# Kernel optimization log

Hardware: AMD Instinct MI355X
Metric: run time of the kernel (lower is better)

Reference implementation:

```python
import jax, jax.numpy as jnp
import numpy as np

HEADS = 4
DIM_HEAD = 32
SCALE = DIM_HEAD ** -0.5
EPS = 1e-5


def setup_inputs() -> dict:
    key = jax.random.key(0)
    k1, k2, k3, k4 = jax.random.split(key, 4)
    dim = 256
    hidden = HEADS * DIM_HEAD  # 128
    x = jax.random.normal(k1, (16, dim, 64, 64), dtype=jnp.float32)
    # 1x1 conv weights stored as [out_ch, in_ch] (kernel size 1 squeezed)
    w_qkv = jax.random.normal(k2, (hidden * 3, dim), dtype=jnp.float32) * (dim ** -0.5)
    w_out = jax.random.normal(k3, (dim, hidden), dtype=jnp.float32) * (hidden ** -0.5)
    b_out = jax.random.normal(k4, (dim,), dtype=jnp.float32) * 0.01
    g = jnp.ones((1, dim, 1, 1), dtype=jnp.float32)  # LayerNorm gain
    return {"x": x, "w_qkv": w_qkv, "w_out": w_out, "b_out": b_out, "g": g}


def reference(x, w_qkv, w_out, b_out, g):
    b, c, h, w = x.shape
    n = h * w
    # 1x1 conv to qkv: [b, 3*hidden, h, w]
    qkv = jnp.einsum('oc,bchw->bohw', w_qkv, x)
    q, k, v = jnp.split(qkv, 3, axis=1)

    def to_heads(t):
        return t.reshape(b, HEADS, DIM_HEAD, n)  # b h d n

    q, k, v = to_heads(q), to_heads(k), to_heads(v)
    q = jax.nn.softmax(q, axis=2) * SCALE       # softmax over head-dim d
    k = jax.nn.softmax(k, axis=3)               # softmax over spatial n
    v = v / n                                    # v / (h*w)
    context = jnp.einsum('bhdn,bhen->bhde', k, v)
    out = jnp.einsum('bhde,bhdn->bhen', context, q)  # b h e n
    out = out.reshape(b, HEADS * DIM_HEAD, h, w)
    # output 1x1 conv with bias
    out = jnp.einsum('oc,bchw->bohw', w_out, out) + b_out[None, :, None, None]
    # channel LayerNorm (biased variance over dim=1)
    mean = jnp.mean(out, axis=1, keepdims=True)
    var = jnp.var(out, axis=1, keepdims=True)
    return (out - mean) * jax.lax.rsqrt(var + EPS) * g
```

## Files before the change

kernel.cpp:

```cpp
#include <hip/hip_runtime.h>

typedef short short8 __attribute__((ext_vector_type(8)));
typedef float f32x16 __attribute__((ext_vector_type(16)));
typedef unsigned short ushort_t;

#define B_    16
#define C_    256
#define N_    4096
#define H_    4
#define HID_  128
#define SCALE_ 0.17677669529663687f
#define EPS_  1e-5f

__device__ inline ushort_t f2bf(float f) {
  union { float f; unsigned u; } a; a.f = f;
  unsigned r = a.u + 0x7FFFu + ((a.u >> 16) & 1u);
  return (ushort_t)(r >> 16);
}

__device__ inline int2 pack4(float a, float b, float c, float d) {
  int2 o;
  o.x = (int)f2bf(a) | ((int)f2bf(b) << 16);
  o.y = (int)f2bf(c) | ((int)f2bf(d) << 16);
  return o;
}

__device__ inline short8 ld_frag16(const ushort_t* p) {
  return __builtin_bit_cast(short8, *(const int4*)p);
}
__device__ inline short8 ld_frag8(const ushort_t* p) {
  int2 a = *(const int2*)p, b = *(const int2*)(p + 4);
  int4 t; t.x = a.x; t.y = a.y; t.z = b.x; t.w = b.y;
  return __builtin_bit_cast(short8, t);
}

__global__ void k0_wswz(const float* __restrict__ w, ushort_t* __restrict__ wsw) {
  int gid = blockIdx.x * 256 + threadIdx.x;
  int ln = gid & 63, kc = (gid >> 6) & 15, mt = gid >> 10;
  int row = mt * 32 + (ln & 31);
  int col = kc * 16 + (ln >> 5) * 8;
  const float* src = w + (size_t)row * 256 + col;
  float4 a = *(const float4*)src, b = *(const float4*)(src + 4);
  union { ushort_t u[8]; int4 v; } o;
  o.u[0] = f2bf(a.x); o.u[1] = f2bf(a.y); o.u[2] = f2bf(a.z); o.u[3] = f2bf(a.w);
  o.u[4] = f2bf(b.x); o.u[5] = f2bf(b.y); o.u[6] = f2bf(b.z); o.u[7] = f2bf(b.w);
  *(int4*)(wsw + (size_t)gid * 8) = o.v;
}

__global__ __launch_bounds__(512, 4) void k1_qkv(
    const float* __restrict__ x, const ushort_t* __restrict__ wsw,
    ushort_t* __restrict__ qp, float* __restrict__ pctx, float* __restrict__ psum)
{
  __shared__ __align__(16) union {
    ushort_t Xs[64 * 264];
    struct { ushort_t kt[128 * 68]; ushort_t vt[128 * 68]; } s2;
  } sm;

  const int tid = threadIdx.x;
  const int b = blockIdx.y;
  const int blk = blockIdx.x;
  const int n0 = blk * 64;
  const int w = tid >> 6, lane = tid & 63;
  const int half = lane >> 5, lm = lane & 31;
  const int hw = w >> 1, ntile = w & 1;
  const int gnt = blk * 2 + ntile;

  {
    const float* xsrc = x + (size_t)b * C_ * N_ + n0;
    const int n4 = tid & 15;
    const int cqA = tid >> 4;
    const int cqB = cqA + 32;
    const float* pA = xsrc + (size_t)(cqA * 4) * N_ + n4 * 4;
    const float* pB = xsrc + (size_t)(cqB * 4) * N_ + n4 * 4;
    float4 a0 = *(const float4*)(pA);
    float4 a1 = *(const float4*)(pA + N_);
    float4 a2 = *(const float4*)(pA + 2 * N_);
    float4 a3 = *(const float4*)(pA + 3 * N_);
    float4 b0 = *(const float4*)(pB);
    float4 b1 = *(const float4*)(pB + N_);
    float4 b2 = *(const float4*)(pB + 2 * N_);
    float4 b3 = *(const float4*)(pB + 3 * N_);
    ushort_t* dA = sm.Xs + (((cqA >> 1) ^ n4) * 8 + (cqA & 1) * 4) + (n4 * 4) * 264;
    ushort_t* dB = sm.Xs + (((cqB >> 1) ^ n4) * 8 + (cqB & 1) * 4) + (n4 * 4) * 264;
    *(int2*)(dA + 0 * 264) = pack4(a0.x, a1.x, a2.x, a3.x);
    *(int2*)(dA + 1 * 264) = pack4(a0.y, a1.y, a2.y, a3.y);
    *(int2*)(dA + 2 * 264) = pack4(a0.z, a1.z, a2.z, a3.z);
    *(int2*)(dA + 3 * 264) = pack4(a0.w, a1.w, a2.w, a3.w);
    *(int2*)(dB + 0 * 264) = pack4(b0.x, b1.x, b2.x, b3.x);
    *(int2*)(dB + 1 * 264) = pack4(b0.y, b1.y, b2.y, b3.y);
    *(int2*)(dB + 2 * 264) = pack4(b0.z, b1.z, b2.z, b3.z);
    *(int2*)(dB + 3 * 264) = pack4(b0.w, b1.w, b2.w, b3.w);
  }
  __syncthreads();

  f32x16 acc0, acc1, acc2;
  for (int r = 0; r < 16; ++r) { acc0[r] = 0.0f; acc1[r] = 0.0f; acc2[r] = 0.0f; }
  {
    const ushort_t* xrow = sm.Xs + (ntile * 32 + lm) * 264;
    const int sn = ntile * 8 + (lm >> 2);
    for (int kc = 0; kc < 16; ++kc) {
      short8 bfrag = ld_frag16(xrow + (((2 * kc + half) ^ sn) << 3));
      short8 af0 = ld_frag16(wsw + (size_t)(((hw) * 16 + kc) * 64 + lane) * 8);
      short8 af1 = ld_frag16(wsw + (size_t)(((4 + hw) * 16 + kc) * 64 + lane) * 8);
      short8 af2 = ld_frag16(wsw + (size_t)(((8 + hw) * 16 + kc) * 64 + lane) * 8);
      acc0 = __builtin_amdgcn_mfma_f32_32x32x16_bf16(af0, bfrag, acc0, 0, 0, 0);
      acc1 = __builtin_amdgcn_mfma_f32_32x32x16_bf16(af1, bfrag, acc1, 0, 0, 0);
      acc2 = __builtin_amdgcn_mfma_f32_32x32x16_bf16(af2, bfrag, acc2, 0, 0, 0);
    }
  }

  {
    float m = -1e30f;
    for (int r = 0; r < 16; ++r) m = fmaxf(m, acc0[r]);
    m = fmaxf(m, __shfl_xor(m, 32));
    float s = 0.0f;
    for (int r = 0; r < 16; ++r) s += __expf(acc0[r] - m);
    s += __shfl_xor(s, 32);
    float sc = SCALE_ / s;
    ushort_t* qpb = qp + (size_t)b * N_ * 128;
    for (int q = 0; q < 4; ++q) {
      int kc = hw * 2 + (q >> 1);
      int fl = (q & 1) * 32 + lm;
      float v0 = __expf(acc0[q * 4 + 0] - m) * sc;
      float v1 = __expf(acc0[q * 4 + 1] - m) * sc;
      float v2 = __expf(acc0[q * 4 + 2] - m) * sc;
      float v3 = __expf(acc0[q * 4 + 3] - m) * sc;
      int2 o;
      o.x = (int)f2bf(v0) | ((int)f2bf(v1) << 16);
      o.y = (int)f2bf(v2) | ((int)f2bf(v3) << 16);
      *(int2*)(qpb + (size_t)((gnt * 8 + kc) * 64 + fl) * 8 + 4 * half) = o;
    }
  }

  float ev[16];
  for (int r = 0; r < 16; ++r) ev[r] = __expf(acc1[r]);

  __syncthreads();

  for (int r = 0; r < 16; ++r) {
    int row = (r & 3) + 8 * (r >> 2) + 4 * half;
    sm.s2.kt[(hw * 32 + row) * 68 + ntile * 32 + lm] = f2bf(ev[r]);
    sm.s2.vt[(hw * 32 + row) * 68 + ntile * 32 + lm] = f2bf(acc2[r]);
  }

  for (int mask = 1; mask <= 16; mask <<= 1)
    for (int r = 0; r < 16; ++r) ev[r] += __shfl_xor(ev[r], mask);
  if (lm == 0) {
    float* ps = psum + ((size_t)(b * 4 + hw) * 128 + gnt) * 32;
    for (int r = 0; r < 16; ++r) {
      int row = (r & 3) + 8 * (r >> 2) + 4 * half;
      ps[row] = ev[r];
    }
  }
  __syncthreads();

  if (ntile == 0) {
    f32x16 cacc;
    for (int r = 0; r < 16; ++r) cacc[r] = 0.0f;
    const ushort_t* ka = sm.s2.kt + (hw * 32 + lm) * 68 + half * 8;
    const ushort_t* va = sm.s2.vt + (hw * 32 + lm) * 68 + half * 8;
    for (int s = 0; s < 4; ++s) {
      short8 af = ld_frag8(ka + s * 16);
      short8 bf = ld_frag8(va + s * 16);
      cacc = __builtin_amdgcn_mfma_f32_32x32x16_bf16(af, bf, cacc, 0, 0, 0);
    }
    float* pc = pctx + ((size_t)(b * 4 + hw) * 64 + blk) * 1024;
    for (int r = 0; r < 16; ++r) {
      int row = (r & 3) + 8 * (r >> 2) + 4 * half;
      pc[row * 32 + lm] = cacc[r];
    }
  }
}

__global__ __launch_bounds__(256) void k2b_weff(
    const float* __restrict__ pctx, const float* __restrict__ psum,
    const float* __restrict__ wout, ushort_t* __restrict__ weff)
{
  __shared__ float ctxs[32][32];
  __shared__ float inv[32];
  const int tid = threadIdx.x;
  const int ph = blockIdx.x, pb = blockIdx.y;
  const size_t bh = (size_t)(pb * 4 + ph);
  if (tid < 32) {
    float s = 0.0f;
    const float* ps = psum + bh * 128 * 32 + tid;
    #pragma unroll 8
    for (int c = 0; c < 128; ++c) s += ps[c * 32];
    inv[tid] = 1.0f / (s * 4096.0f);
  }
  __syncthreads();
  {
    float4 s4 = make_float4(0.f, 0.f, 0.f, 0.f);
    const float* pc = pctx + bh * 64 * 1024 + tid * 4;
    #pragma unroll 8
    for (int c = 0; c < 64; ++c) {
      float4 v = *(const float4*)(pc + c * 1024);
      s4.x += v.x; s4.y += v.y; s4.z += v.z; s4.w += v.w;
    }
    int d = tid >> 3;
    float iv = inv[d];
    float* crow = &ctxs[0][0] + tid * 4;
    crow[0] = s4.x * iv; crow[1] = s4.y * iv; crow[2] = s4.z * iv; crow[3] = s4.w * iv;
  }
  __syncthreads();
  {
    const int oc = tid;
    const int mt = oc >> 5, lmm = oc & 31;
    const float* wrow = wout + (size_t)oc * HID_ + ph * 32;
    float wr[32];
    for (int e = 0; e < 32; ++e) wr[e] = wrow[e];
    float vals[32];
    for (int d = 0; d < 32; ++d) {
      float s = 0.0f;
      for (int e = 0; e < 32; ++e) s += wr[e] * ctxs[d][e];
      vals[d] = s;
    }
    ushort_t* wb_b = weff + (size_t)pb * 32768;
    for (int kci = 0; kci < 2; ++kci) {
      int kc = ph * 2 + kci;
      for (int hf = 0; hf < 2; ++hf) {
        int d0 = kci * 16 + hf * 8;
        union { ushort_t u[8]; int4 v; } o;
        for (int j = 0; j < 8; ++j) o.u[j] = f2bf(vals[d0 + j]);
        *(int4*)(wb_b + (size_t)((mt * 8 + kc) * 64 + hf * 32 + lmm) * 8) = o.v;
      }
    }
  }
}

__global__ __launch_bounds__(256, 4) void k3_out(
    const ushort_t* __restrict__ weff, const ushort_t* __restrict__ qp,
    const float* __restrict__ bout, const float* __restrict__ g,
    float* __restrict__ out)
{
  __shared__ float part_s[2][64], part_s2[2][64];
  __shared__ float st_mu[64], st_rs[64];

  const int tid = threadIdx.x;
  const int b = blockIdx.y;
  const int blk = blockIdx.x;
  const int n0 = blk * 64;
  const int w = tid >> 6, lane = tid & 63;
  const int half = lane >> 5, lm = lane & 31;
  const int ntile = w & 1, mgrp = w >> 1;
  const int gnt = blk * 2 + ntile;

  f32x16 acc[4];
  for (int i = 0; i < 4; ++i)
    for (int r = 0; r < 16; ++r) acc[i][r] = 0.0f;

  {
    const ushort_t* qb = qp + (size_t)b * N_ * 128 + (size_t)gnt * 8 * 64 * 8;
    const ushort_t* wbase = weff + (size_t)b * 32768 + ((size_t)(mgrp * 4) * 8 * 64 + lane) * 8;
    for (int kc = 0; kc < 8; ++kc) {
      short8 bfrag = ld_frag16(qb + (size_t)(kc * 64 + lane) * 8);
      for (int i = 0; i < 4; ++i) {
        short8 af = ld_frag16(wbase + (size_t)((i * 8 + kc) * 64) * 8);
        acc[i] = __builtin_amdgcn_mfma_f32_32x32x16_bf16(af, bfrag, acc[i], 0, 0, 0);
      }
    }
  }

  float s = 0.0f, s2v = 0.0f;
  for (int i = 0; i < 4; ++i) {
    int mt = mgrp * 4 + i;
    for (int r = 0; r < 16; ++r) {
      int row = mt * 32 + (r & 3) + 8 * (r >> 2) + 4 * half;
      acc[i][r] += bout[row];
      float v = acc[i][r];
      s += v; s2v += v * v;
    }
  }
  s += __shfl_xor(s, 32);
  s2v += __shfl_xor(s2v, 32);
  if (half == 0) { part_s[mgrp][ntile * 32 + lm] = s; part_s2[mgrp][ntile * 32 + lm] = s2v; }
  __syncthreads();
  if (tid < 64) {
    float S = part_s[0][tid] + part_s[1][tid];
    float S2 = part_s2[0][tid] + part_s2[1][tid];
    float mu = S * (1.0f / 256.0f);
    float var = S2 * (1.0f / 256.0f) - mu * mu;
    st_mu[tid] = mu;
    st_rs[tid] = rsqrtf(var + EPS_);
  }
  __syncthreads();

  const int col = ntile * 32 + lm;
  const float mu = st_mu[col];
  const float rs = st_rs[col];
  float* ob = out + (size_t)b * C_ * N_ + n0 + col;
  for (int i = 0; i < 4; ++i) {
    int mt = mgrp * 4 + i;
    for (int r = 0; r < 16; ++r) {
      int row = mt * 32 + (r & 3) + 8 * (r >> 2) + 4 * half;
      ob[(size_t)row * N_] = (acc[i][r] - mu) * rs * g[row];
    }
  }
}

extern "C" void kernel_launch(void* const* d_in, const int* in_sizes, int n_in,
                              void* d_out, int out_size, void* d_ws, size_t ws_size,
                              hipStream_t stream) {
  (void)in_sizes; (void)n_in; (void)out_size; (void)ws_size;
  const float* x    = (const float*)d_in[0];
  const float* wqkv = (const float*)d_in[1];
  const float* wout = (const float*)d_in[2];
  const float* bout = (const float*)d_in[3];
  const float* g    = (const float*)d_in[4];
  float* out = (float*)d_out;

  char* ws = (char*)d_ws;
  ushort_t* qp   = (ushort_t*)(ws);
  float*    pctx = (float*)(ws + ((size_t)16 << 20));
  float*    psum = (float*)(ws + ((size_t)32 << 20));
  ushort_t* weff = (ushort_t*)(ws + ((size_t)33 << 20));
  ushort_t* wsw  = (ushort_t*)(ws + ((size_t)34 << 20));

  k0_wswz<<<48, 256, 0, stream>>>(wqkv, wsw);
  k1_qkv<<<dim3(64, 16), 512, 0, stream>>>(x, wsw, qp, pctx, psum);
  k2b_weff<<<dim3(4, 16), 256, 0, stream>>>(pctx, psum, wout, weff);
  k3_out<<<dim3(64, 16), 256, 0, stream>>>(weff, qp, bout, g, out);
}
```

Baseline: 168.0 us.

## Reduce context and key sums with global atomics and software-pipeline QKV loads

```diff
diff --git a/kernel.cpp b/kernel.cpp
--- a/kernel.cpp
+++ b/kernel.cpp
@@ -34,8 +34,16 @@
   return __builtin_bit_cast(short8, t);
 }
 
-__global__ void k0_wswz(const float* __restrict__ w, ushort_t* __restrict__ wsw) {
+__global__ void k0_wswz(const float* __restrict__ w, ushort_t* __restrict__ wsw,
+                        float* __restrict__ ctxg, float* __restrict__ psumg) {
   int gid = blockIdx.x * 256 + threadIdx.x;
+  #pragma unroll
+  for (int i = 0; i < 6; ++i) {
+    int idx = gid + i * 12288;
+    if (idx < 65536) ctxg[idx] = 0.0f;
+  }
+  if (gid < 2048) psumg[gid] = 0.0f;
+
   int ln = gid & 63, kc = (gid >> 6) & 15, mt = gid >> 10;
   int row = mt * 32 + (ln & 31);
   int col = kc * 16 + (ln >> 5) * 8;
@@ -49,7 +57,7 @@
 
 __global__ __launch_bounds__(512, 4) void k1_qkv(
     const float* __restrict__ x, const ushort_t* __restrict__ wsw,
-    ushort_t* __restrict__ qp, float* __restrict__ pctx, float* __restrict__ psum)
+    ushort_t* __restrict__ qp, float* __restrict__ ctxg, float* __restrict__ psumg)
 {
   __shared__ __align__(16) union {
     ushort_t Xs[64 * 264];
@@ -98,36 +106,46 @@
   {
     const ushort_t* xrow = sm.Xs + (ntile * 32 + lm) * 264;
     const int sn = ntile * 8 + (lm >> 2);
+    const ushort_t* wl = wsw + (size_t)(hw * 16 * 64 + lane) * 8;
+
+#define LOADK(kc, BF, A0, A1, A2) \
+    BF = ld_frag16(xrow + (((2 * (kc) + half) ^ sn) << 3)); \
+    A0 = ld_frag16(wl + (kc) * 512); \
+    A1 = ld_frag16(wl + 32768 + (kc) * 512); \
+    A2 = ld_frag16(wl + 65536 + (kc) * 512);
+
+    short8 cb, c0, c1, c2, nb, n0f, n1f, n2f;
+    LOADK(0, cb, c0, c1, c2);
+    LOADK(1, nb, n0f, n1f, n2f);
+    #pragma unroll
     for (int kc = 0; kc < 16; ++kc) {
-      short8 bfrag = ld_frag16(xrow + (((2 * kc + half) ^ sn) << 3));
-      short8 af0 = ld_frag16(wsw + (size_t)(((hw) * 16 + kc) * 64 + lane) * 8);
-      short8 af1 = ld_frag16(wsw + (size_t)(((4 + hw) * 16 + kc) * 64 + lane) * 8);
-      short8 af2 = ld_frag16(wsw + (size_t)(((8 + hw) * 16 + kc) * 64 + lane) * 8);
-      acc0 = __builtin_amdgcn_mfma_f32_32x32x16_bf16(af0, bfrag, acc0, 0, 0, 0);
-      acc1 = __builtin_amdgcn_mfma_f32_32x32x16_bf16(af1, bfrag, acc1, 0, 0, 0);
-      acc2 = __builtin_amdgcn_mfma_f32_32x32x16_bf16(af2, bfrag, acc2, 0, 0, 0);
-    }
+      short8 tb, t0, t1, t2;
+      if (kc < 14) { LOADK(kc + 2, tb, t0, t1, t2); }
+      else { tb = cb; t0 = c0; t1 = c1; t2 = c2; }
+      acc0 = __builtin_amdgcn_mfma_f32_32x32x16_bf16(c0, cb, acc0, 0, 0, 0);
+      acc1 = __builtin_amdgcn_mfma_f32_32x32x16_bf16(c1, cb, acc1, 0, 0, 0);
+      acc2 = __builtin_amdgcn_mfma_f32_32x32x16_bf16(c2, cb, acc2, 0, 0, 0);
+      cb = nb; c0 = n0f; c1 = n1f; c2 = n2f;
+      nb = tb; n0f = t0; n1f = t1; n2f = t2;
+    }
+#undef LOADK
   }
 
   {
     float m = -1e30f;
     for (int r = 0; r < 16; ++r) m = fmaxf(m, acc0[r]);
     m = fmaxf(m, __shfl_xor(m, 32));
+    float qe[16];
     float s = 0.0f;
-    for (int r = 0; r < 16; ++r) s += __expf(acc0[r] - m);
+    for (int r = 0; r < 16; ++r) { qe[r] = __expf(acc0[r] - m); s += qe[r]; }
     s += __shfl_xor(s, 32);
     float sc = SCALE_ / s;
     ushort_t* qpb = qp + (size_t)b * N_ * 128;
     for (int q = 0; q < 4; ++q) {
       int kc = hw * 2 + (q >> 1);
       int fl = (q & 1) * 32 + lm;
-      float v0 = __expf(acc0[q * 4 + 0] - m) * sc;
-      float v1 = __expf(acc0[q * 4 + 1] - m) * sc;
-      float v2 = __expf(acc0[q * 4 + 2] - m) * sc;
-      float v3 = __expf(acc0[q * 4 + 3] - m) * sc;
-      int2 o;
-      o.x = (int)f2bf(v0) | ((int)f2bf(v1) << 16);
-      o.y = (int)f2bf(v2) | ((int)f2bf(v3) << 16);
+      int2 o = pack4(qe[q * 4 + 0] * sc, qe[q * 4 + 1] * sc,
+                     qe[q * 4 + 2] * sc, qe[q * 4 + 3] * sc);
       *(int2*)(qpb + (size_t)((gnt * 8 + kc) * 64 + fl) * 8 + 4 * half) = o;
     }
   }
@@ -142,38 +160,40 @@
     sm.s2.kt[(hw * 32 + row) * 68 + ntile * 32 + lm] = f2bf(ev[r]);
     sm.s2.vt[(hw * 32 + row) * 68 + ntile * 32 + lm] = f2bf(acc2[r]);
   }
-
-  for (int mask = 1; mask <= 16; mask <<= 1)
-    for (int r = 0; r < 16; ++r) ev[r] += __shfl_xor(ev[r], mask);
-  if (lm == 0) {
-    float* ps = psum + ((size_t)(b * 4 + hw) * 128 + gnt) * 32;
-    for (int r = 0; r < 16; ++r) {
-      int row = (r & 3) + 8 * (r >> 2) + 4 * half;
-      ps[row] = ev[r];
-    }
-  }
-  __syncthreads();
-
-  if (ntile == 0) {
-    f32x16 cacc;
-    for (int r = 0; r < 16; ++r) cacc[r] = 0.0f;
-    const ushort_t* ka = sm.s2.kt + (hw * 32 + lm) * 68 + half * 8;
-    const ushort_t* va = sm.s2.vt + (hw * 32 + lm) * 68 + half * 8;
-    for (int s = 0; s < 4; ++s) {
+  __syncthreads();
+
+  {
+    f32x16 cacc, sacc;
+    for (int r = 0; r < 16; ++r) { cacc[r] = 0.0f; sacc[r] = 0.0f; }
+    short8 ones;
+    #pragma unroll
+    for (int j = 0; j < 8; ++j) ones[j] = (short)0x3F80;
+    const ushort_t* ka = sm.s2.kt + (hw * 32 + lm) * 68 + ntile * 32 + half * 8;
+    const ushort_t* va = sm.s2.vt + (hw * 32 + lm) * 68 + ntile * 32 + half * 8;
+    #pragma unroll
+    for (int s = 0; s < 2; ++s) {
       short8 af = ld_frag8(ka + s * 16);
       short8 bf = ld_frag8(va + s * 16);
       cacc = __builtin_amdgcn_mfma_f32_32x32x16_bf16(af, bf, cacc, 0, 0, 0);
-    }
-    float* pc = pctx + ((size_t)(b * 4 + hw) * 64 + blk) * 1024;
+      sacc = __builtin_amdgcn_mfma_f32_32x32x16_bf16(af, ones, sacc, 0, 0, 0);
+    }
+    float* pc = ctxg + (size_t)(b * 4 + hw) * 1024;
     for (int r = 0; r < 16; ++r) {
       int row = (r & 3) + 8 * (r >> 2) + 4 * half;
-      pc[row * 32 + lm] = cacc[r];
+      atomicAdd(pc + row * 32 + lm, cacc[r]);
+    }
+    if (lm == 0) {
+      float* ps = psumg + (size_t)(b * 4 + hw) * 32;
+      for (int r = 0; r < 16; ++r) {
+        int row = (r & 3) + 8 * (r >> 2) + 4 * half;
+        atomicAdd(ps + row, sacc[r]);
+      }
     }
   }
 }
 
 __global__ __launch_bounds__(256) void k2b_weff(
-    const float* __restrict__ pctx, const float* __restrict__ psum,
+    const float* __restrict__ ctxg, const float* __restrict__ psumg,
     const float* __restrict__ wout, ushort_t* __restrict__ weff)
 {
   __shared__ float ctxs[32][32];
@@ -181,26 +201,13 @@
   const int tid = threadIdx.x;
   const int ph = blockIdx.x, pb = blockIdx.y;
   const size_t bh = (size_t)(pb * 4 + ph);
-  if (tid < 32) {
-    float s = 0.0f;
-    const float* ps = psum + bh * 128 * 32 + tid;
-    #pragma unroll 8
-    for (int c = 0; c < 128; ++c) s += ps[c * 32];
-    inv[tid] = 1.0f / (s * 4096.0f);
-  }
-  __syncthreads();
-  {
-    float4 s4 = make_float4(0.f, 0.f, 0.f, 0.f);
-    const float* pc = pctx + bh * 64 * 1024 + tid * 4;
-    #pragma unroll 8
-    for (int c = 0; c < 64; ++c) {
-      float4 v = *(const float4*)(pc + c * 1024);
-      s4.x += v.x; s4.y += v.y; s4.z += v.z; s4.w += v.w;
-    }
-    int d = tid >> 3;
-    float iv = inv[d];
+  float4 v = *(const float4*)(ctxg + bh * 1024 + tid * 4);
+  if (tid < 32) inv[tid] = 1.0f / (psumg[bh * 32 + tid] * 4096.0f);
+  __syncthreads();
+  {
+    float iv = inv[tid >> 3];
     float* crow = &ctxs[0][0] + tid * 4;
-    crow[0] = s4.x * iv; crow[1] = s4.y * iv; crow[2] = s4.z * iv; crow[3] = s4.w * iv;
+    crow[0] = v.x * iv; crow[1] = v.y * iv; crow[2] = v.z * iv; crow[3] = v.w * iv;
   }
   __syncthreads();
   {
@@ -311,13 +318,13 @@
 
   char* ws = (char*)d_ws;
   ushort_t* qp   = (ushort_t*)(ws);
-  float*    pctx = (float*)(ws + ((size_t)16 << 20));
-  float*    psum = (float*)(ws + ((size_t)32 << 20));
-  ushort_t* weff = (ushort_t*)(ws + ((size_t)33 << 20));
-  ushort_t* wsw  = (ushort_t*)(ws + ((size_t)34 << 20));
-
-  k0_wswz<<<48, 256, 0, stream>>>(wqkv, wsw);
-  k1_qkv<<<dim3(64, 16), 512, 0, stream>>>(x, wsw, qp, pctx, psum);
-  k2b_weff<<<dim3(4, 16), 256, 0, stream>>>(pctx, psum, wout, weff);
+  ushort_t* weff = (ushort_t*)(ws + ((size_t)16 << 20));
+  ushort_t* wsw  = (ushort_t*)(ws + ((size_t)17 << 20));
+  float*    ctxg = (float*)(ws + ((size_t)18 << 20));
+  float*    psumg= (float*)(ws + ((size_t)18 << 20) + (256 << 10));
+
+  k0_wswz<<<48, 256, 0, stream>>>(wqkv, wsw, ctxg, psumg);
+  k1_qkv<<<dim3(64, 16), 512, 0, stream>>>(x, wsw, qp, ctxg, psumg);
+  k2b_weff<<<dim3(4, 16), 256, 0, stream>>>(ctxg, psumg, wout, weff);
   k3_out<<<dim3(64, 16), 256, 0, stream>>>(weff, qp, bout, g, out);
 }
```

Measured after the change: 230.2 us. 37.1% more time.

## Split partial context reduction into a separate wide-grid kernel, cache q exponentials

Applied to the files above, without the earlier changes.

```diff
diff --git a/kernel.cpp b/kernel.cpp
--- a/kernel.cpp
+++ b/kernel.cpp
@@ -113,21 +113,17 @@
     float m = -1e30f;
     for (int r = 0; r < 16; ++r) m = fmaxf(m, acc0[r]);
     m = fmaxf(m, __shfl_xor(m, 32));
+    float qe[16];
     float s = 0.0f;
-    for (int r = 0; r < 16; ++r) s += __expf(acc0[r] - m);
+    for (int r = 0; r < 16; ++r) { qe[r] = __expf(acc0[r] - m); s += qe[r]; }
     s += __shfl_xor(s, 32);
     float sc = SCALE_ / s;
     ushort_t* qpb = qp + (size_t)b * N_ * 128;
     for (int q = 0; q < 4; ++q) {
       int kc = hw * 2 + (q >> 1);
       int fl = (q & 1) * 32 + lm;
-      float v0 = __expf(acc0[q * 4 + 0] - m) * sc;
-      float v1 = __expf(acc0[q * 4 + 1] - m) * sc;
-      float v2 = __expf(acc0[q * 4 + 2] - m) * sc;
-      float v3 = __expf(acc0[q * 4 + 3] - m) * sc;
-      int2 o;
-      o.x = (int)f2bf(v0) | ((int)f2bf(v1) << 16);
-      o.y = (int)f2bf(v2) | ((int)f2bf(v3) << 16);
+      int2 o = pack4(qe[q * 4 + 0] * sc, qe[q * 4 + 1] * sc,
+                     qe[q * 4 + 2] * sc, qe[q * 4 + 3] * sc);
       *(int2*)(qpb + (size_t)((gnt * 8 + kc) * 64 + fl) * 8 + 4 * half) = o;
     }
   }
@@ -172,8 +168,39 @@
   }
 }
 
+__global__ __launch_bounds__(256) void kr_reduce(
+    const float* __restrict__ pctx, const float* __restrict__ psum,
+    float* __restrict__ ctxr, float* __restrict__ psumr)
+{
+  __shared__ float red[8][32];
+  const int tid = threadIdx.x;
+  const int q = blockIdx.x;
+  const int bh = blockIdx.y;
+  const int idx = q * 256 + tid;
+  const float* src = pctx + (size_t)bh * 65536 + idx;
+  float s = 0.0f;
+  #pragma unroll 8
+  for (int blk = 0; blk < 64; ++blk) s += src[blk * 1024];
+  ctxr[(size_t)bh * 1024 + idx] = s;
+  if (q == 0) {
+    const int d = tid & 31, part = tid >> 5;
+    const float* ps = psum + (size_t)bh * 4096 + part * 512 + d;
+    float t = 0.0f;
+    #pragma unroll
+    for (int g = 0; g < 16; ++g) t += ps[g * 32];
+    red[part][d] = t;
+    __syncthreads();
+    if (tid < 32) {
+      float u = 0.0f;
+      #pragma unroll
+      for (int p = 0; p < 8; ++p) u += red[p][tid];
+      psumr[(size_t)bh * 32 + tid] = u;
+    }
+  }
+}
+
 __global__ __launch_bounds__(256) void k2b_weff(
-    const float* __restrict__ pctx, const float* __restrict__ psum,
+    const float* __restrict__ ctxr, const float* __restrict__ psumr,
     const float* __restrict__ wout, ushort_t* __restrict__ weff)
 {
   __shared__ float ctxs[32][32];
@@ -181,26 +208,13 @@
   const int tid = threadIdx.x;
   const int ph = blockIdx.x, pb = blockIdx.y;
   const size_t bh = (size_t)(pb * 4 + ph);
-  if (tid < 32) {
-    float s = 0.0f;
-    const float* ps = psum + bh * 128 * 32 + tid;
-    #pragma unroll 8
-    for (int c = 0; c < 128; ++c) s += ps[c * 32];
-    inv[tid] = 1.0f / (s * 4096.0f);
-  }
-  __syncthreads();
-  {
-    float4 s4 = make_float4(0.f, 0.f, 0.f, 0.f);
-    const float* pc = pctx + bh * 64 * 1024 + tid * 4;
-    #pragma unroll 8
-    for (int c = 0; c < 64; ++c) {
-      float4 v = *(const float4*)(pc + c * 1024);
-      s4.x += v.x; s4.y += v.y; s4.z += v.z; s4.w += v.w;
-    }
-    int d = tid >> 3;
-    float iv = inv[d];
+  float4 v = *(const float4*)(ctxr + bh * 1024 + tid * 4);
+  if (tid < 32) inv[tid] = 1.0f / (psumr[bh * 32 + tid] * 4096.0f);
+  __syncthreads();
+  {
+    float iv = inv[tid >> 3];
     float* crow = &ctxs[0][0] + tid * 4;
-    crow[0] = s4.x * iv; crow[1] = s4.y * iv; crow[2] = s4.z * iv; crow[3] = s4.w * iv;
+    crow[0] = v.x * iv; crow[1] = v.y * iv; crow[2] = v.z * iv; crow[3] = v.w * iv;
   }
   __syncthreads();
   {
@@ -310,14 +324,17 @@
   float* out = (float*)d_out;
 
   char* ws = (char*)d_ws;
-  ushort_t* qp   = (ushort_t*)(ws);
-  float*    pctx = (float*)(ws + ((size_t)16 << 20));
-  float*    psum = (float*)(ws + ((size_t)32 << 20));
-  ushort_t* weff = (ushort_t*)(ws + ((size_t)33 << 20));
-  ushort_t* wsw  = (ushort_t*)(ws + ((size_t)34 << 20));
+  ushort_t* qp    = (ushort_t*)(ws);
+  float*    pctx  = (float*)(ws + ((size_t)16 << 20));
+  float*    psum  = (float*)(ws + ((size_t)32 << 20));
+  ushort_t* weff  = (ushort_t*)(ws + ((size_t)33 << 20));
+  ushort_t* wsw   = (ushort_t*)(ws + ((size_t)34 << 20));
+  float*    ctxr  = (float*)(ws + ((size_t)34 << 20) + (192 << 10));
+  float*    psumr = (float*)(ws + ((size_t)34 << 20) + (448 << 10));
 
   k0_wswz<<<48, 256, 0, stream>>>(wqkv, wsw);
   k1_qkv<<<dim3(64, 16), 512, 0, stream>>>(x, wsw, qp, pctx, psum);
-  k2b_weff<<<dim3(4, 16), 256, 0, stream>>>(pctx, psum, wout, weff);
+  kr_reduce<<<dim3(4, 64), 256, 0, stream>>>(pctx, psum, ctxr, psumr);
+  k2b_weff<<<dim3(4, 16), 256, 0, stream>>>(ctxr, psumr, wout, weff);
   k3_out<<<dim3(64, 16), 256, 0, stream>>>(weff, qp, bout, g, out);
 }
```

New measurement: 165.9 us. About the same (-1.2%).
